# Optimization experiments

Measured on AMD Instinct MI355X. Metric: run time of the kernel, lower is better.

Reference implementation:

```python
import jax, jax.numpy as jnp
import numpy as np

N_TRAIN = 131072
M_TEST = 65536
T_SPAN = 100.0
D = 3  # Matern-5/2 state dim


def setup_inputs() -> dict:
    key = jax.random.key(0)
    k1, k2, k3, k4 = jax.random.split(key, 4)
    times = jnp.sort(jax.random.uniform(k1, (N_TRAIN,), jnp.float32) * T_SPAN)
    t_star = jnp.sort(jax.random.uniform(k2, (M_TEST,), jnp.float32) * T_SPAN)
    # positive site precisions, site naturals scaled so pseudo-targets are O(1)
    site_nat2 = jax.random.uniform(k3, (N_TRAIN,), jnp.float32) * 4.0 + 0.5
    site_nat1 = jax.random.normal(k4, (N_TRAIN,), jnp.float32) * site_nat2
    return dict(
        times=times,
        t_star=t_star,
        site_nat1=site_nat1,
        site_nat2=site_nat2,
        variance=jnp.float32(1.0),
        lengthscale=jnp.float32(0.5),
        mean_const=jnp.float32(0.1),
    )


def _matern52_sde(variance, lengthscale):
    lam = jnp.sqrt(5.0).astype(jnp.float32) / lengthscale
    F = jnp.array([[0.0, 1.0, 0.0],
                   [0.0, 0.0, 1.0],
                   [0.0, 0.0, 0.0]], jnp.float32)
    F = F.at[2, 0].set(-lam ** 3).at[2, 1].set(-3.0 * lam ** 2).at[2, 2].set(-3.0 * lam)
    kappa = lam ** 2 / 3.0
    P_inf = variance * jnp.array([[1.0, 0.0, 0.0],
                                  [0.0, 0.0, 0.0],
                                  [0.0, 0.0, 0.0]], jnp.float32)
    P_inf = P_inf.at[0, 2].set(-variance * kappa)
    P_inf = P_inf.at[2, 0].set(-variance * kappa)
    P_inf = P_inf.at[1, 1].set(variance * kappa)
    P_inf = P_inf.at[2, 2].set(variance * lam ** 4)
    H = jnp.array([[1.0, 0.0, 0.0]], jnp.float32)
    return F, H, P_inf, lam


def _discretise(F, P_inf, lam, dt):
    # (F + lam I) is nilpotent of index 3 -> exact expm
    I = jnp.eye(D, dtype=jnp.float32)
    Nm = F + lam * I
    Nm2 = Nm @ Nm
    dt_ = dt[:, None, None]
    A = jnp.exp(-lam * dt)[:, None, None] * (I + dt_ * Nm + 0.5 * dt_ ** 2 * Nm2)
    APA = jnp.einsum('tij,jk,tlk->til', A, P_inf, A)
    Q = P_inf - APA
    return A, Q


def _kalman_filter(H, P_inf, A_seq, Q_seq, residual, is_obs, R_full):
    h = H[0]  # [D]

    def step(carry, inp):
        m, P = carry
        A, Q, r, obs, R = inp
        m_pred = A @ m
        P_pred = A @ P @ A.T + Q
        S = h @ P_pred @ h + R
        K = obs * (P_pred @ h) / S  # masked gain: test points skip update
        v = r - m_pred @ h
        m_f = m_pred + K * v
        P_f = P_pred - jnp.outer(K, K) * S
        return (m_f, P_f), (m_pred, P_pred, m_f, P_f)

    init = (jnp.zeros(D, jnp.float32), P_inf)
    _, (m_pred, P_pred, m_filt, P_filt) = jax.lax.scan(
        step, init, (A_seq, Q_seq, residual, is_obs, R_full))
    return m_pred, P_pred, m_filt, P_filt


def _rts_smoother(m_pred, P_pred, m_filt, P_filt, A_seq):
    def back(carry, inp):
        m_s_next, P_s_next = carry
        m_f, P_f, A_n, m_p_n, P_p_n = inp
        G = jnp.linalg.solve(P_p_n, A_n @ P_f).T  # P_f A^T P_pred^{-1}
        m_s = m_f + G @ (m_s_next - m_p_n)
        P_s = P_f + G @ (P_s_next - P_p_n) @ G.T
        return (m_s, P_s), (m_s, P_s)

    init = (m_filt[-1], P_filt[-1])
    xs = (m_filt[:-1], P_filt[:-1], A_seq[1:], m_pred[1:], P_pred[1:])
    _, (m_s, P_s) = jax.lax.scan(back, init, xs, reverse=True)
    m_smooth = jnp.concatenate([m_s, m_filt[-1:]], axis=0)
    P_smooth = jnp.concatenate([P_s, P_filt[-1:]], axis=0)
    return m_smooth, P_smooth


def reference(times, t_star, site_nat1, site_nat2, variance, lengthscale, mean_const):
    F, H, P_inf, lam = _matern52_sde(variance, lengthscale)
    N = times.shape[0]
    M = t_star.shape[0]
    merged = jnp.concatenate([times, t_star])
    order = jnp.argsort(merged)  # jnp.argsort is stable
    merged_sorted = merged[order]
    is_obs = jnp.concatenate([jnp.ones(N, jnp.float32), jnp.zeros(M, jnp.float32)])[order]
    pseudo_targets = site_nat1 / site_nat2
    residual_full = jnp.concatenate([pseudo_targets - mean_const,
                                     jnp.zeros(M, jnp.float32)])[order]
    R_full = jnp.concatenate([jnp.reciprocal(site_nat2), jnp.ones(M, jnp.float32)])[order]
    dt_full = jnp.concatenate([jnp.zeros(1, jnp.float32), jnp.diff(merged_sorted)])
    A_seq, Q_seq = _discretise(F, P_inf, lam, dt_full)
    m_pred, P_pred, m_filt, P_filt = _kalman_filter(
        H, P_inf, A_seq, Q_seq, residual_full, is_obs, R_full)
    m_smooth, P_smooth = _rts_smoother(m_pred, P_pred, m_filt, P_filt, A_seq)
    inv_order = jnp.argsort(order)
    test_positions = inv_order[N:]
    m_test = m_smooth[test_positions]
    P_test = P_smooth[test_positions]
    means = m_test @ H[0] + mean_const  # H = [1,0,0]
    vars_ = jnp.einsum('i,tij,j->t', H[0], P_test, H[0])
    return means, jnp.maximum(vars_, 0.0)
```

## Files before the change

kernel.cpp:

```cpp
#include <hip/hip_runtime.h>
#include <math.h>

#define DEV __device__ __forceinline__

constexpr int N_TRAIN = 131072;
constexpr int M_TEST  = 65536;
constexpr int T_TOT   = N_TRAIN + M_TEST;
constexpr int TPB     = 64;
constexpr int NBLK    = T_TOT / TPB;
constexpr int GRP     = 64;
constexpr int NGRP    = NBLK / GRP;
constexpr int FE_S    = 33;

DEV void mm(const float* X, const float* Y, float* Z) {
#pragma unroll
  for (int i = 0; i < 3; ++i)
#pragma unroll
    for (int j = 0; j < 3; ++j)
      Z[i*3+j] = X[i*3]*Y[j] + X[i*3+1]*Y[3+j] + X[i*3+2]*Y[6+j];
}
DEV void mmnt(const float* X, const float* Y, float* Z) {
#pragma unroll
  for (int i = 0; i < 3; ++i)
#pragma unroll
    for (int j = 0; j < 3; ++j)
      Z[i*3+j] = X[i*3]*Y[j*3] + X[i*3+1]*Y[j*3+1] + X[i*3+2]*Y[j*3+2];
}
DEV void mtn(const float* X, const float* Y, float* Z) {
#pragma unroll
  for (int i = 0; i < 3; ++i)
#pragma unroll
    for (int j = 0; j < 3; ++j)
      Z[i*3+j] = X[i]*Y[j] + X[3+i]*Y[3+j] + X[6+i]*Y[6+j];
}
DEV void mv(const float* X, const float* v, float* w) {
#pragma unroll
  for (int i = 0; i < 3; ++i) w[i] = X[i*3]*v[0] + X[i*3+1]*v[1] + X[i*3+2]*v[2];
}
DEV void mtv(const float* X, const float* v, float* w) {
#pragma unroll
  for (int i = 0; i < 3; ++i) w[i] = X[i]*v[0] + X[3+i]*v[1] + X[6+i]*v[2];
}
DEV void inv3(const float* mf_, float* o) {
  double m0=mf_[0], m1=mf_[1], m2=mf_[2], m3=mf_[3], m4=mf_[4],
         m5=mf_[5], m6=mf_[6], m7=mf_[7], m8=mf_[8];
  double c00 = m4*m8 - m5*m7;
  double c10 = m5*m6 - m3*m8;
  double c20 = m3*m7 - m4*m6;
  double det = m0*c00 + m1*c10 + m2*c20;
  double id = 1.0 / det;
  o[0] = (float)(c00*id); o[1] = (float)((m2*m7-m1*m8)*id); o[2] = (float)((m1*m5-m2*m4)*id);
  o[3] = (float)(c10*id); o[4] = (float)((m0*m8-m2*m6)*id); o[5] = (float)((m2*m3-m0*m5)*id);
  o[6] = (float)(c20*id); o[7] = (float)((m1*m6-m0*m7)*id); o[8] = (float)((m0*m4-m1*m3)*id);
}
DEV void symm(float* P) {
  float a = 0.5f*(P[1]+P[3]), b = 0.5f*(P[2]+P[6]), c = 0.5f*(P[5]+P[7]);
  P[1]=P[3]=a; P[2]=P[6]=b; P[5]=P[7]=c;
}

struct Model { float lam, v, kap, l4; };
DEV Model make_model(const float* varp, const float* ellp) {
  Model M; M.v = varp[0];
  float ell = ellp[0];
  M.lam = sqrtf(5.0f) / ell;
  M.kap = M.lam * M.lam / 3.0f;
  float l2 = M.lam * M.lam;
  M.l4 = l2 * l2;
  return M;
}
DEV void pinf(const Model& M, float* P) {
  float vk = M.v * M.kap;
  P[0]=M.v; P[1]=0;  P[2]=-vk;
  P[3]=0;   P[4]=vk; P[5]=0;
  P[6]=-vk; P[7]=0;  P[8]=M.v*M.l4;
}
DEV void make_AQ(const Model& M, float dt, float* A, float* Q) {
  float lam = M.lam, l2 = lam*lam, l3 = l2*lam, l4 = M.l4;
  float e = __expf(-lam * dt);
  float h = 0.5f * dt * dt;
  A[0] = e*(1.0f + dt*lam + h*l2);
  A[1] = e*(dt + 2.0f*h*lam);
  A[2] = e*h;
  A[3] = e*(-h*l3);
  A[4] = e*(1.0f + dt*lam - 2.0f*h*l2);
  A[5] = e*(dt - h*lam);
  A[6] = e*(-dt*l3 + h*l4);
  A[7] = e*(-3.0f*dt*l2 + 2.0f*h*l3);
  A[8] = e*(1.0f - 2.0f*dt*lam + h*l2);
  float vk = M.v * M.kap, vl4 = M.v * M.l4;
  float B[9];
#pragma unroll
  for (int i = 0; i < 3; ++i) {
    B[i*3+0] =  A[i*3+0]*M.v - A[i*3+2]*vk;
    B[i*3+1] =  A[i*3+1]*vk;
    B[i*3+2] = -A[i*3+0]*vk  + A[i*3+2]*vl4;
  }
  float Pi[9]; pinf(M, Pi);
#pragma unroll
  for (int i = 0; i < 3; ++i)
#pragma unroll
    for (int j = 0; j < 3; ++j)
      Q[i*3+j] = Pi[i*3+j] - (B[i*3]*A[j*3] + B[i*3+1]*A[j*3+1] + B[i*3+2]*A[j*3+2]);
}

struct FE { float A[9]; float b[3]; float C[9]; float h[3]; float J[9]; };

DEV FE fe_identity() {
  FE e;
#pragma unroll
  for (int i=0;i<9;++i){ e.A[i]=0.0f; e.C[i]=0.0f; e.J[i]=0.0f; }
  e.A[0]=e.A[4]=e.A[8]=1.0f;
  e.b[0]=e.b[1]=e.b[2]=0.0f; e.h[0]=e.h[1]=e.h[2]=0.0f;
  return e;
}
DEV void fe_store(const FE& e, float* g) {
#pragma unroll
  for (int i=0;i<9;++i) g[i]=e.A[i];
  g[9]=e.b[0]; g[10]=e.b[1]; g[11]=e.b[2];
#pragma unroll
  for (int i=0;i<9;++i) g[12+i]=e.C[i];
  g[21]=e.h[0]; g[22]=e.h[1]; g[23]=e.h[2];
#pragma unroll
  for (int i=0;i<9;++i) g[24+i]=e.J[i];
}
DEV FE fe_load(const float* g) {
  FE e;
#pragma unroll
  for (int i=0;i<9;++i) e.A[i]=g[i];
  e.b[0]=g[9]; e.b[1]=g[10]; e.b[2]=g[11];
#pragma unroll
  for (int i=0;i<9;++i) e.C[i]=g[12+i];
  e.h[0]=g[21]; e.h[1]=g[22]; e.h[2]=g[23];
#pragma unroll
  for (int i=0;i<9;++i) e.J[i]=g[24+i];
  return e;
}
DEV void fe_storeT(const FE& e, float* g, int idx, int n) {
#pragma unroll
  for (int i=0;i<9;++i) g[i*n+idx]=e.A[i];
#pragma unroll
  for (int i=0;i<3;++i) g[(9+i)*n+idx]=e.b[i];
#pragma unroll
  for (int i=0;i<9;++i) g[(12+i)*n+idx]=e.C[i];
#pragma unroll
  for (int i=0;i<3;++i) g[(21+i)*n+idx]=e.h[i];
#pragma unroll
  for (int i=0;i<9;++i) g[(24+i)*n+idx]=e.J[i];
}
DEV FE fe_loadT(const float* g, int idx, int n) {
  FE e;
#pragma unroll
  for (int i=0;i<9;++i) e.A[i]=g[i*n+idx];
#pragma unroll
  for (int i=0;i<3;++i) e.b[i]=g[(9+i)*n+idx];
#pragma unroll
  for (int i=0;i<9;++i) e.C[i]=g[(12+i)*n+idx];
#pragma unroll
  for (int i=0;i<3;++i) e.h[i]=g[(21+i)*n+idx];
#pragma unroll
  for (int i=0;i<9;++i) e.J[i]=g[(24+i)*n+idx];
  return e;
}
DEV FE fe_shfl_up(const FE& e, int d) {
  FE o;
#pragma unroll
  for (int i=0;i<9;++i) o.A[i]=__shfl_up(e.A[i], d, 64);
#pragma unroll
  for (int i=0;i<3;++i) o.b[i]=__shfl_up(e.b[i], d, 64);
#pragma unroll
  for (int i=0;i<9;++i) o.C[i]=__shfl_up(e.C[i], d, 64);
#pragma unroll
  for (int i=0;i<3;++i) o.h[i]=__shfl_up(e.h[i], d, 64);
#pragma unroll
  for (int i=0;i<9;++i) o.J[i]=__shfl_up(e.J[i], d, 64);
  return o;
}
DEV FE build_felem(const Model& M, float dt, float obsf, float rf, float Rf_, bool first) {
  FE E;
  float r = rf, R = Rf_;
  float g = (obsf > 0.5f) ? 1.0f : 0.0f;
  if (first) {
#pragma unroll
    for (int i=0;i<9;++i){ E.A[i]=0.0f; E.J[i]=0.0f; }
    E.h[0]=E.h[1]=E.h[2]=0.0f;
    float Pi[9]; pinf(M, Pi);
    float S = Pi[0] + R;
    float f = g / S;
    float K0=Pi[0]*f, K1=Pi[3]*f, K2=Pi[6]*f;
    E.b[0]=K0*r; E.b[1]=K1*r; E.b[2]=K2*r;
    E.C[0]=Pi[0]-S*K0*K0; E.C[1]=Pi[1]-S*K0*K1; E.C[2]=Pi[2]-S*K0*K2;
    E.C[3]=Pi[3]-S*K1*K0; E.C[4]=Pi[4]-S*K1*K1; E.C[5]=Pi[5]-S*K1*K2;
    E.C[6]=Pi[6]-S*K2*K0; E.C[7]=Pi[7]-S*K2*K1; E.C[8]=Pi[8]-S*K2*K2;
    return E;
  }
  float Am[9], Q[9]; make_AQ(M, dt, Am, Q);
  float S = Q[0] + R, iS = g / S;
  float K0=Q[0]*iS, K1=Q[3]*iS, K2=Q[6]*iS;
#pragma unroll
  for (int j = 0; j < 3; ++j) {
    E.A[j]   = Am[j]   - K0*Am[j];
    E.A[3+j] = Am[3+j] - K1*Am[j];
    E.A[6+j] = Am[6+j] - K2*Am[j];
    E.C[j]   = Q[j]    - K0*Q[j];
    E.C[3+j] = Q[3+j]  - K1*Q[j];
    E.C[6+j] = Q[6+j]  - K2*Q[j];
  }
  E.b[0]=K0*r; E.b[1]=K1*r; E.b[2]=K2*r;
  float riS = r*iS;
  E.h[0]=Am[0]*riS; E.h[1]=Am[1]*riS; E.h[2]=Am[2]*riS;
#pragma unroll
  for (int i = 0; i < 3; ++i)
#pragma unroll
    for (int j = 0; j < 3; ++j)
      E.J[i*3+j] = Am[i]*Am[j]*iS;
  return E;
}
DEV FE fcompose(const FE& x, const FE& y) {
  const float *A1=x.A,*b1=x.b,*C1=x.C,*h1=x.h,*J1=x.J;
  const float *A2=y.A,*b2=y.b,*C2=y.C,*h2=y.h,*J2=y.J;
  FE o;
  float Mx[9]; mm(C1,J2,Mx); Mx[0]+=1.0f; Mx[4]+=1.0f; Mx[8]+=1.0f;
  float Mi[9]; inv3(Mx,Mi);
  float T1[9]; mm(A2,Mi,T1);
  mm(T1,A1,o.A);
  float u[3]; mv(C1,h2,u); u[0]+=b1[0]; u[1]+=b1[1]; u[2]+=b1[2];
  mv(T1,u,o.b); o.b[0]+=b2[0]; o.b[1]+=b2[1]; o.b[2]+=b2[2];
  float t2[9]; mm(T1,C1,t2);
  mmnt(t2,A2,o.C);
#pragma unroll
  for (int i=0;i<9;++i) o.C[i]+=C2[i];
  float tmp[9]; mm(Mi,A1,tmp);
  float w[3]; mv(J2,b1,w);
  w[0]=h2[0]-w[0]; w[1]=h2[1]-w[1]; w[2]=h2[2]-w[2];
  mtv(tmp,w,o.h); o.h[0]+=h1[0]; o.h[1]+=h1[1]; o.h[2]+=h1[2];
  float V[9]; mm(J2,A1,V);
  mtn(tmp,V,o.J);
#pragma unroll
  for (int i=0;i<9;++i) o.J[i]+=J1[i];
  symm(o.C); symm(o.J);
  return o;
}
DEV void fstep(const Model& M, float dt, float obsf, float rf, float Rf_,
               float* m, float* P) {
  float A[9], Q[9]; make_AQ(M, dt, A, Q);
  float mp[3]; mv(A, m, mp);
  float W[9]; mmnt(P, A, W);
  float Pp[9]; mm(A, W, Pp);
#pragma unroll
  for (int i=0;i<9;++i) Pp[i]+=Q[i];
  float S = Pp[0] + Rf_;
  float f = (obsf > 0.5f) ? (1.0f/S) : 0.0f;
  float K0=Pp[0]*f, K1=Pp[3]*f, K2=Pp[6]*f;
  float v = rf - mp[0];
  m[0]=mp[0]+K0*v; m[1]=mp[1]+K1*v; m[2]=mp[2]+K2*v;
  P[0]=Pp[0]-S*K0*K0; P[1]=Pp[1]-S*K0*K1; P[2]=Pp[2]-S*K0*K2;
  P[3]=Pp[3]-S*K1*K0; P[4]=Pp[4]-S*K1*K1; P[5]=Pp[5]-S*K1*K2;
  P[6]=Pp[6]-S*K2*K0; P[7]=Pp[7]-S*K2*K1; P[8]=Pp[8]-S*K2*K2;
  symm(P);
}

struct SE { float G[9]; float c[3]; float U[9]; };

DEV SE se_identity() {
  SE s;
#pragma unroll
  for (int i=0;i<9;++i){ s.G[i]=0.0f; s.U[i]=0.0f; }
  s.G[0]=s.G[4]=s.G[8]=1.0f;
  s.c[0]=s.c[1]=s.c[2]=0.0f;
  return s;
}
DEV void se_store(const SE& s, float* g) {
#pragma unroll
  for (int i=0;i<9;++i) g[i]=s.G[i];
  g[9]=s.c[0]; g[10]=s.c[1]; g[11]=s.c[2];
  g[12]=s.U[0]; g[13]=s.U[1]; g[14]=s.U[2]; g[15]=s.U[4]; g[16]=s.U[5]; g[17]=s.U[8];
}
DEV SE se_load(const float* g) {
  SE s;
#pragma unroll
  for (int i=0;i<9;++i) s.G[i]=g[i];
  s.c[0]=g[9]; s.c[1]=g[10]; s.c[2]=g[11];
  s.U[0]=g[12]; s.U[1]=g[13]; s.U[2]=g[14];
  s.U[3]=g[13]; s.U[4]=g[15]; s.U[5]=g[16];
  s.U[6]=g[14]; s.U[7]=g[16]; s.U[8]=g[17];
  return s;
}
DEV void se_storeT(const SE& s, float* g, int idx, int n) {
#pragma unroll
  for (int i=0;i<9;++i) g[i*n+idx]=s.G[i];
#pragma unroll
  for (int i=0;i<3;++i) g[(9+i)*n+idx]=s.c[i];
  g[12*n+idx]=s.U[0]; g[13*n+idx]=s.U[1]; g[14*n+idx]=s.U[2];
  g[15*n+idx]=s.U[4]; g[16*n+idx]=s.U[5]; g[17*n+idx]=s.U[8];
}
DEV SE se_loadT(const float* g, int idx, int n) {
  SE s;
#pragma unroll
  for (int i=0;i<9;++i) s.G[i]=g[i*n+idx];
#pragma unroll
  for (int i=0;i<3;++i) s.c[i]=g[(9+i)*n+idx];
  float u0=g[12*n+idx], u1=g[13*n+idx], u2=g[14*n+idx],
        u4=g[15*n+idx], u5=g[16*n+idx], u8=g[17*n+idx];
  s.U[0]=u0; s.U[1]=u1; s.U[2]=u2;
  s.U[3]=u1; s.U[4]=u4; s.U[5]=u5;
  s.U[6]=u2; s.U[7]=u5; s.U[8]=u8;
  return s;
}
DEV SE se_shfl_down(const SE& s, int d) {
  SE o;
#pragma unroll
  for (int i=0;i<9;++i) o.G[i]=__shfl_down(s.G[i], d, 64);
#pragma unroll
  for (int i=0;i<3;++i) o.c[i]=__shfl_down(s.c[i], d, 64);
#pragma unroll
  for (int i=0;i<9;++i) o.U[i]=__shfl_down(s.U[i], d, 64);
  return o;
}
DEV SE scompose(const SE& x, const SE& y) {
  SE o;
  mm(x.G, y.G, o.G);
  float t[3]; mv(x.G, y.c, t);
  o.c[0]=t[0]+x.c[0]; o.c[1]=t[1]+x.c[1]; o.c[2]=t[2]+x.c[2];
  float T[9]; mm(x.G, y.U, T);
  mmnt(T, x.G, o.U);
#pragma unroll
  for (int i=0;i<9;++i) o.U[i]+=x.U[i];
  symm(o.U);
  return o;
}
DEV void sapply(const SE& s, float* m, float* P) {
  float t[3]; mv(s.G, m, t);
  float T[9]; mm(s.G, P, T);
  float Pn[9]; mmnt(T, s.G, Pn);
  m[0]=t[0]+s.c[0]; m[1]=t[1]+s.c[1]; m[2]=t[2]+s.c[2];
#pragma unroll
  for (int i=0;i<9;++i) P[i]=Pn[i]+s.U[i];
  symm(P);
}
DEV SE build_selem(const Model& M, const float4* pk, const float* mf, const float* Pf, int k) {
  float m[3] = { mf[k], mf[T_TOT+k], mf[2*T_TOT+k] };
  float p00=Pf[k], p01=Pf[T_TOT+k], p02=Pf[2*T_TOT+k],
        p11=Pf[3*T_TOT+k], p12=Pf[4*T_TOT+k], p22=Pf[5*T_TOT+k];
  float P[9] = { p00,p01,p02, p01,p11,p12, p02,p12,p22 };
  float dt = pk[k+1].x - pk[k].x;
  SE s;
  float A[9], Q[9]; make_AQ(M, dt, A, Q);
  float W[9]; mmnt(P, A, W);
  float Pp[9]; mm(A, W, Pp);
#pragma unroll
  for (int j=0;j<9;++j) Pp[j]+=Q[j];
  float Pi_[9]; inv3(Pp, Pi_);
  mm(W, Pi_, s.G);
  float mp[3]; mv(A, m, mp);
  float gm[3]; mv(s.G, mp, gm);
  s.c[0]=m[0]-gm[0]; s.c[1]=m[1]-gm[1]; s.c[2]=m[2]-gm[2];
  float GW[9]; mmnt(s.G, W, GW);
#pragma unroll
  for (int j=0;j<9;++j) s.U[j]=P[j]-GW[j];
  symm(s.U);
  return s;
}

__global__ void k_merge(const float* __restrict__ times, const float* __restrict__ tstar,
                        const float* __restrict__ n1, const float* __restrict__ n2,
                        const float* __restrict__ mcp,
                        float4* pk, int* oix) {
  int g = blockIdx.x*blockDim.x + threadIdx.x;
  if (g >= T_TOT) return;
  float mc = mcp[0];
  if (g < N_TRAIN) {
    int i = g;
    float t = times[i];
    int lo = 0, hi = M_TEST;
    while (lo < hi) { int mid=(lo+hi)>>1; if (tstar[mid] < t) lo=mid+1; else hi=mid; }
    int p = i + lo;
    float s2 = n2[i];
    pk[p] = make_float4(t, n1[i]/s2 - mc, 1.0f/s2, 1.0f);
    oix[p] = -1;
  } else {
    int j = g - N_TRAIN;
    float t = tstar[j];
    int lo = 0, hi = N_TRAIN;
    while (lo < hi) { int mid=(lo+hi)>>1; if (times[mid] <= t) lo=mid+1; else hi=mid; }
    int p = j + lo;
    pk[p] = make_float4(t, 0.f, 1.f, 0.f);
    oix[p] = j;
  }
}

__global__ __launch_bounds__(TPB, 3) void k_f1(
    const float* varp, const float* ellp, const float4* __restrict__ pk,
    float* tIncl, float* blkAgg) {
  int l = threadIdx.x, b = blockIdx.x;
  int t = b*TPB + l;
  Model M = make_model(varp, ellp);
  float4 q = pk[t];
  float dt = (t == 0) ? 0.0f : (q.x - pk[t-1].x);
  FE run = build_felem(M, dt, q.w, q.y, q.z, t == 0);
  for (int d = 1; d < TPB; d <<= 1) {
    FE oth = fe_shfl_up(run, d);
    FE comp = fcompose(oth, run);
    if (l >= d) run = comp;
  }
  fe_storeT(run, tIncl, t, T_TOT);
  if (l == TPB-1) fe_storeT(run, blkAgg, b, NBLK);
}

__global__ __launch_bounds__(TPB, 2) void k_f2a(const float* __restrict__ blkAgg,
                                                float* blkIncl2, float* grpAgg) {
  int l = threadIdx.x, gb = blockIdx.x;
  int b = gb*GRP + l;
  FE run = fe_loadT(blkAgg, b, NBLK);
  for (int d = 1; d < TPB; d <<= 1) {
    FE oth = fe_shfl_up(run, d);
    FE comp = fcompose(oth, run);
    if (l >= d) run = comp;
  }
  fe_storeT(run, blkIncl2, b, NBLK);
  if (l == GRP-1) fe_store(run, grpAgg + gb*FE_S);
}

__global__ __launch_bounds__(TPB, 2) void k_f2b(const float* __restrict__ grpAgg,
                                                float* grpPref) {
  int j = threadIdx.x;
  FE run = (j < NGRP) ? fe_load(grpAgg + j*FE_S) : fe_identity();
  for (int d = 1; d < TPB; d <<= 1) {
    FE oth = fe_shfl_up(run, d);
    FE comp = fcompose(oth, run);
    if (j >= d) run = comp;
  }
  FE X = fe_shfl_up(run, 1);
  if (j < NGRP) {
    if (j == 0) X = fe_identity();
    fe_store(X, grpPref + j*FE_S);
  }
}

__global__ __launch_bounds__(TPB, 3) void k_f3(
    const float* varp, const float* ellp, const float4* __restrict__ pk,
    const float* __restrict__ tIncl, const float* __restrict__ blkIncl2,
    const float* __restrict__ grpPref,
    float* mf, float* Pf, float* xT) {
  int l = threadIdx.x, b = blockIdx.x;
  int t = b*TPB + l;
  int g = b >> 6, lb = b & (GRP-1);
  Model M = make_model(varp, ellp);
  float m[3], P[9];
  if (t == 0) {
    m[0]=m[1]=m[2]=0.0f; pinf(M, P);
  } else {
    FE gp = fe_load(grpPref + g*FE_S);
    FE entB = (lb == 0) ? gp : fcompose(gp, fe_loadT(blkIncl2, b-1, NBLK));
    FE ent  = (l == 0) ? entB : fcompose(entB, fe_loadT(tIncl, t-1, T_TOT));
    m[0]=ent.b[0]; m[1]=ent.b[1]; m[2]=ent.b[2];
#pragma unroll
    for (int i=0;i<9;++i) P[i]=ent.C[i];
  }
  float4 q = pk[t];
  float dt = (t == 0) ? 0.0f : (q.x - pk[t-1].x);
  fstep(M, dt, q.w, q.y, q.z, m, P);
  mf[t]=m[0]; mf[T_TOT+t]=m[1]; mf[2*T_TOT+t]=m[2];
  Pf[t]=P[0]; Pf[T_TOT+t]=P[1]; Pf[2*T_TOT+t]=P[2];
  Pf[3*T_TOT+t]=P[4]; Pf[4*T_TOT+t]=P[5]; Pf[5*T_TOT+t]=P[8];
  if (t == T_TOT-1) {
    xT[0]=m[0]; xT[1]=m[1]; xT[2]=m[2];
    xT[3]=P[0]; xT[4]=P[1]; xT[5]=P[2];
    xT[6]=P[4]; xT[7]=P[5]; xT[8]=P[8];
  }
}

__global__ __launch_bounds__(TPB, 3) void k_s1(
    const float* varp, const float* ellp, const float4* __restrict__ pk,
    const float* __restrict__ mf, const float* __restrict__ Pf,
    float* eSel, float* tSuf, float* blkAggS) {
  int l = threadIdx.x, b = blockIdx.x;
  int t = b*TPB + l;
  Model M = make_model(varp, ellp);
  SE e = (t <= T_TOT-2) ? build_selem(M, pk, mf, Pf, t) : se_identity();
  se_storeT(e, eSel, t, T_TOT);
  SE Macc = e;
  for (int d = 1; d < TPB; d <<= 1) {
    SE oth = se_shfl_down(Macc, d);
    SE comp = scompose(Macc, oth);
    if (l + d < TPB) Macc = comp;
  }
  se_storeT(Macc, tSuf, t, T_TOT);
  if (l == 0) se_storeT(Macc, blkAggS, b, NBLK);
}

__global__ __launch_bounds__(TPB, 2) void k_s2a(const float* __restrict__ blkAggS,
                                                float* blkSuf2, float* grpAggS) {
  int l = threadIdx.x, gb = blockIdx.x;
  int b = gb*GRP + l;
  SE run = se_loadT(blkAggS, b, NBLK);
  for (int d = 1; d < TPB; d <<= 1) {
    SE oth = se_shfl_down(run, d);
    SE comp = scompose(run, oth);
    if (l + d < TPB) run = comp;
  }
  se_storeT(run, blkSuf2, b, NBLK);
  if (l == 0) se_store(run, grpAggS + gb*18);
}

__global__ __launch_bounds__(TPB, 2) void k_s2b(const float* __restrict__ grpAggS,
                                                const float* __restrict__ xT,
                                                float* gExit) {
  int j = threadIdx.x;
  SE run = (j < NGRP) ? se_load(grpAggS + j*18) : se_identity();
  for (int d = 1; d < TPB; d <<= 1) {
    SE oth = se_shfl_down(run, d);
    SE comp = scompose(run, oth);
    if (j + d < TPB) run = comp;
  }
  SE Sx = se_shfl_down(run, 1);
  if (j < NGRP) {
    float m[3] = { xT[0], xT[1], xT[2] };
    float P[9] = { xT[3],xT[4],xT[5], xT[4],xT[6],xT[7], xT[5],xT[7],xT[8] };
    if (j < NGRP-1) sapply(Sx, m, P);
    float* o = gExit + j*9;
    o[0]=m[0];o[1]=m[1];o[2]=m[2];o[3]=P[0];o[4]=P[1];o[5]=P[2];o[6]=P[4];o[7]=P[5];o[8]=P[8];
  }
}

__global__ __launch_bounds__(TPB, 4) void k_s3(
    const float* mcp,
    const float* __restrict__ eSel, const float* __restrict__ tSuf,
    const float* __restrict__ blkSuf2, const float* __restrict__ gExit,
    const int* __restrict__ oix, float* out) {
  int l = threadIdx.x, b = blockIdx.x;
  int t = b*TPB + l;
  int g = b >> 6, lb = b & (GRP-1);
  float mc = mcp[0];
  const float* ge = gExit + g*9;
  float m[3] = { ge[0], ge[1], ge[2] };
  float P[9] = { ge[3],ge[4],ge[5], ge[4],ge[6],ge[7], ge[5],ge[7],ge[8] };
  if (lb < GRP-1) {
    SE s = se_loadT(blkSuf2, b+1, NBLK);
    sapply(s, m, P);
  }
  if (l < TPB-1) {
    SE s = se_loadT(tSuf, t+1, T_TOT);
    sapply(s, m, P);
  }
  {
    SE e = se_loadT(eSel, t, T_TOT);
    sapply(e, m, P);
  }
  int j = oix[t];
  if (j >= 0) { out[j] = m[0] + mc; out[M_TEST + j] = fmaxf(P[0], 0.0f); }
}

extern "C" void kernel_launch(void* const* d_in, const int* in_sizes, int n_in,
                              void* d_out, int out_size, void* d_ws, size_t ws_size,
                              hipStream_t stream) {
  const float* times = (const float*)d_in[0];
  const float* tstar = (const float*)d_in[1];
  const float* n1    = (const float*)d_in[2];
  const float* n2    = (const float*)d_in[3];
  const float* varp  = (const float*)d_in[4];
  const float* ellp  = (const float*)d_in[5];
  const float* mcp   = (const float*)d_in[6];
  float* out = (float*)d_out;

  size_t off = 0;
  auto take = [&](size_t bytes) {
    char* p = (char*)d_ws + off;
    off += (bytes + 255) & ~(size_t)255;
    return (void*)p;
  };
  float4* pk     = (float4*)take(sizeof(float4) * T_TOT);
  int*    oix    = (int*)   take(sizeof(int)    * T_TOT);
  float*  mf     = (float*) take(sizeof(float)  * 3 * T_TOT);
  float*  Pf     = (float*) take(sizeof(float)  * 6 * T_TOT);
  float*  tIncl  = (float*) take(sizeof(float)  * FE_S * T_TOT);
  float*  blkAgg = (float*) take(sizeof(float)  * FE_S * NBLK);
  float*  blkIncl2=(float*) take(sizeof(float)  * FE_S * NBLK);
  float*  grpAgg = (float*) take(sizeof(float)  * FE_S * NGRP);
  float*  grpPref= (float*) take(sizeof(float)  * FE_S * NGRP);
  float*  eSel   = (float*) take(sizeof(float)  * 18 * T_TOT);
  float*  tSuf   = (float*) take(sizeof(float)  * 18 * T_TOT);
  float*  blkAggS= (float*) take(sizeof(float)  * 18 * NBLK);
  float*  blkSuf2= (float*) take(sizeof(float)  * 18 * NBLK);
  float*  grpAggS= (float*) take(sizeof(float)  * 18 * NGRP);
  float*  gExit  = (float*) take(sizeof(float)  * 9  * NGRP);
  float*  xT     = (float*) take(sizeof(float)  * 9);
  (void)ws_size; (void)in_sizes; (void)n_in; (void)out_size;

  k_merge<<<(T_TOT+255)/256, 256, 0, stream>>>(times, tstar, n1, n2, mcp, pk, oix);
  k_f1   <<<NBLK, TPB, 0, stream>>>(varp, ellp, pk, tIncl, blkAgg);
  k_f2a  <<<NGRP, TPB, 0, stream>>>(blkAgg, blkIncl2, grpAgg);
  k_f2b  <<<1, TPB, 0, stream>>>(grpAgg, grpPref);
  k_f3   <<<NBLK, TPB, 0, stream>>>(varp, ellp, pk, tIncl, blkIncl2, grpPref, mf, Pf, xT);
  k_s1   <<<NBLK, TPB, 0, stream>>>(varp, ellp, pk, mf, Pf, eSel, tSuf, blkAggS);
  k_s2a  <<<NGRP, TPB, 0, stream>>>(blkAggS, blkSuf2, grpAggS);
  k_s2b  <<<1, TPB, 0, stream>>>(grpAggS, xT, gExit);
  k_s3   <<<NBLK, TPB, 0, stream>>>(mcp, eSel, tSuf, blkSuf2, gExit, oix, out);
}
```

Baseline: 150.5 us.

## Fuse smoother element build into filter pass and apply prefixes to state directly

Smoother elements are now built inside the final filter kernel from the just-computed filtered state, so the filtered means and covariances are no longer written to and re-read from global memory by a separate kernel. The filter prefix is applied to the state vector with a cheaper apply routine instead of composing full elements, which avoids up to two full 3x3 compositions per thread. The final smoother step computes only the entries it needs for the mean and variance outputs. The 3x3 inverse inside element composition is switched from double to single precision, which may reduce numerical accuracy.

```diff
diff --git a/kernel.cpp b/kernel.cpp
--- a/kernel.cpp
+++ b/kernel.cpp
@@ -41,7 +41,17 @@
 #pragma unroll
   for (int i = 0; i < 3; ++i) w[i] = X[i]*v[0] + X[3+i]*v[1] + X[6+i]*v[2];
 }
-DEV void inv3(const float* mf_, float* o) {
+DEV void inv3f(const float* m, float* o) {
+  float c00 = m[4]*m[8] - m[5]*m[7];
+  float c10 = m[5]*m[6] - m[3]*m[8];
+  float c20 = m[3]*m[7] - m[4]*m[6];
+  float det = m[0]*c00 + m[1]*c10 + m[2]*c20;
+  float id = 1.0f / det;
+  o[0] = c00*id; o[1] = (m[2]*m[7]-m[1]*m[8])*id; o[2] = (m[1]*m[5]-m[2]*m[4])*id;
+  o[3] = c10*id; o[4] = (m[0]*m[8]-m[2]*m[6])*id; o[5] = (m[2]*m[3]-m[0]*m[5])*id;
+  o[6] = c20*id; o[7] = (m[1]*m[6]-m[0]*m[7])*id; o[8] = (m[0]*m[4]-m[1]*m[3])*id;
+}
+DEV void inv3d(const float* mf_, float* o) {
   double m0=mf_[0], m1=mf_[1], m2=mf_[2], m3=mf_[3], m4=mf_[4],
          m5=mf_[5], m6=mf_[6], m7=mf_[7], m8=mf_[8];
   double c00 = m4*m8 - m5*m7;
@@ -161,6 +171,12 @@
   for (int i=0;i<9;++i) e.J[i]=g[(24+i)*n+idx];
   return e;
 }
+DEV void fe_loadT_state(const float* g, int idx, int n, float* m, float* P) {
+#pragma unroll
+  for (int i=0;i<3;++i) m[i]=g[(9+i)*n+idx];
+#pragma unroll
+  for (int i=0;i<9;++i) P[i]=g[(12+i)*n+idx];
+}
 DEV FE fe_shfl_up(const FE& e, int d) {
   FE o;
 #pragma unroll
@@ -220,7 +236,7 @@
   const float *A2=y.A,*b2=y.b,*C2=y.C,*h2=y.h,*J2=y.J;
   FE o;
   float Mx[9]; mm(C1,J2,Mx); Mx[0]+=1.0f; Mx[4]+=1.0f; Mx[8]+=1.0f;
-  float Mi[9]; inv3(Mx,Mi);
+  float Mi[9]; inv3f(Mx,Mi);
   float T1[9]; mm(A2,Mi,T1);
   mm(T1,A1,o.A);
   float u[3]; mv(C1,h2,u); u[0]+=b1[0]; u[1]+=b1[1]; u[2]+=b1[2];
@@ -239,6 +255,19 @@
   for (int i=0;i<9;++i) o.J[i]+=J1[i];
   symm(o.C); symm(o.J);
   return o;
+}
+DEV void fapply(const FE& y, float* m, float* P) {
+  float Mx[9]; mm(P, y.J, Mx); Mx[0]+=1.0f; Mx[4]+=1.0f; Mx[8]+=1.0f;
+  float Mi[9]; inv3f(Mx, Mi);
+  float T1[9]; mm(y.A, Mi, T1);
+  float u[3]; mv(P, y.h, u); u[0]+=m[0]; u[1]+=m[1]; u[2]+=m[2];
+  float mn[3]; mv(T1, u, mn);
+  m[0]=mn[0]+y.b[0]; m[1]=mn[1]+y.b[1]; m[2]=mn[2]+y.b[2];
+  float t2[9]; mm(T1, P, t2);
+  float Pn[9]; mmnt(t2, y.A, Pn);
+#pragma unroll
+  for (int i=0;i<9;++i) P[i]=Pn[i]+y.C[i];
+  symm(P);
 }
 DEV void fstep(const Model& M, float dt, float obsf, float rf, float Rf_,
                float* m, float* P) {
@@ -337,19 +366,14 @@
   for (int i=0;i<9;++i) P[i]=Pn[i]+s.U[i];
   symm(P);
 }
-DEV SE build_selem(const Model& M, const float4* pk, const float* mf, const float* Pf, int k) {
-  float m[3] = { mf[k], mf[T_TOT+k], mf[2*T_TOT+k] };
-  float p00=Pf[k], p01=Pf[T_TOT+k], p02=Pf[2*T_TOT+k],
-        p11=Pf[3*T_TOT+k], p12=Pf[4*T_TOT+k], p22=Pf[5*T_TOT+k];
-  float P[9] = { p00,p01,p02, p01,p11,p12, p02,p12,p22 };
-  float dt = pk[k+1].x - pk[k].x;
+DEV SE selem_from_state(const Model& M, const float* m, const float* P, float dtn) {
   SE s;
-  float A[9], Q[9]; make_AQ(M, dt, A, Q);
+  float A[9], Q[9]; make_AQ(M, dtn, A, Q);
   float W[9]; mmnt(P, A, W);
   float Pp[9]; mm(A, W, Pp);
 #pragma unroll
   for (int j=0;j<9;++j) Pp[j]+=Q[j];
-  float Pi_[9]; inv3(Pp, Pi_);
+  float Pi_[9]; inv3d(Pp, Pi_);
   mm(W, Pi_, s.G);
   float mp[3]; mv(A, m, mp);
   float gm[3]; mv(s.G, mp, gm);
@@ -440,7 +464,7 @@
     const float* varp, const float* ellp, const float4* __restrict__ pk,
     const float* __restrict__ tIncl, const float* __restrict__ blkIncl2,
     const float* __restrict__ grpPref,
-    float* mf, float* Pf, float* xT) {
+    float* eSel, float* xT) {
   int l = threadIdx.x, b = blockIdx.x;
   int t = b*TPB + l;
   int g = b >> 6, lb = b & (GRP-1);
@@ -448,37 +472,41 @@
   float m[3], P[9];
   if (t == 0) {
     m[0]=m[1]=m[2]=0.0f; pinf(M, P);
+  } else if (g == 0 && lb == 0) {
+    fe_loadT_state(tIncl, t-1, T_TOT, m, P);
+  } else if (g == 0) {
+    fe_loadT_state(blkIncl2, b-1, NBLK, m, P);
+    if (l > 0) { FE y = fe_loadT(tIncl, t-1, T_TOT); fapply(y, m, P); }
   } else {
-    FE gp = fe_load(grpPref + g*FE_S);
-    FE entB = (lb == 0) ? gp : fcompose(gp, fe_loadT(blkIncl2, b-1, NBLK));
-    FE ent  = (l == 0) ? entB : fcompose(entB, fe_loadT(tIncl, t-1, T_TOT));
-    m[0]=ent.b[0]; m[1]=ent.b[1]; m[2]=ent.b[2];
-#pragma unroll
-    for (int i=0;i<9;++i) P[i]=ent.C[i];
+    const float* gp = grpPref + g*FE_S;
+    m[0]=gp[9]; m[1]=gp[10]; m[2]=gp[11];
+#pragma unroll
+    for (int i=0;i<9;++i) P[i]=gp[12+i];
+    if (lb > 0) { FE y = fe_loadT(blkIncl2, b-1, NBLK); fapply(y, m, P); }
+    if (l  > 0) { FE y = fe_loadT(tIncl,  t-1, T_TOT); fapply(y, m, P); }
   }
   float4 q = pk[t];
   float dt = (t == 0) ? 0.0f : (q.x - pk[t-1].x);
   fstep(M, dt, q.w, q.y, q.z, m, P);
-  mf[t]=m[0]; mf[T_TOT+t]=m[1]; mf[2*T_TOT+t]=m[2];
-  Pf[t]=P[0]; Pf[T_TOT+t]=P[1]; Pf[2*T_TOT+t]=P[2];
-  Pf[3*T_TOT+t]=P[4]; Pf[4*T_TOT+t]=P[5]; Pf[5*T_TOT+t]=P[8];
-  if (t == T_TOT-1) {
+  SE e;
+  if (t < T_TOT-1) {
+    float dtn = pk[t+1].x - q.x;
+    e = selem_from_state(M, m, P, dtn);
+  } else {
+    e = se_identity();
     xT[0]=m[0]; xT[1]=m[1]; xT[2]=m[2];
     xT[3]=P[0]; xT[4]=P[1]; xT[5]=P[2];
     xT[6]=P[4]; xT[7]=P[5]; xT[8]=P[8];
   }
-}
-
-__global__ __launch_bounds__(TPB, 3) void k_s1(
-    const float* varp, const float* ellp, const float4* __restrict__ pk,
-    const float* __restrict__ mf, const float* __restrict__ Pf,
-    float* eSel, float* tSuf, float* blkAggS) {
+  se_storeT(e, eSel, t, T_TOT);
+}
+
+__global__ __launch_bounds__(TPB, 4) void k_s1(
+    const float* __restrict__ eSel,
+    float* tSuf, float* blkAggS) {
   int l = threadIdx.x, b = blockIdx.x;
   int t = b*TPB + l;
-  Model M = make_model(varp, ellp);
-  SE e = (t <= T_TOT-2) ? build_selem(M, pk, mf, Pf, t) : se_identity();
-  se_storeT(e, eSel, t, T_TOT);
-  SE Macc = e;
+  SE Macc = se_loadT(eSel, t, T_TOT);
   for (int d = 1; d < TPB; d <<= 1) {
     SE oth = se_shfl_down(Macc, d);
     SE comp = scompose(Macc, oth);
@@ -542,12 +570,15 @@
     SE s = se_loadT(tSuf, t+1, T_TOT);
     sapply(s, m, P);
   }
-  {
-    SE e = se_loadT(eSel, t, T_TOT);
-    sapply(e, m, P);
-  }
+  float g0 = eSel[0*T_TOT+t], g1 = eSel[1*T_TOT+t], g2 = eSel[2*T_TOT+t];
+  float c0 = eSel[9*T_TOT+t], u00 = eSel[12*T_TOT+t];
+  float m0 = g0*m[0] + g1*m[1] + g2*m[2] + c0;
+  float p0 = g0*P[0] + g1*P[3] + g2*P[6];
+  float p1 = g0*P[1] + g1*P[4] + g2*P[7];
+  float p2 = g0*P[2] + g1*P[5] + g2*P[8];
+  float v00 = p0*g0 + p1*g1 + p2*g2 + u00;
   int j = oix[t];
-  if (j >= 0) { out[j] = m[0] + mc; out[M_TEST + j] = fmaxf(P[0], 0.0f); }
+  if (j >= 0) { out[j] = m0 + mc; out[M_TEST + j] = fmaxf(v00, 0.0f); }
 }
 
 extern "C" void kernel_launch(void* const* d_in, const int* in_sizes, int n_in,
@@ -570,8 +601,6 @@
   };
   float4* pk     = (float4*)take(sizeof(float4) * T_TOT);
   int*    oix    = (int*)   take(sizeof(int)    * T_TOT);
-  float*  mf     = (float*) take(sizeof(float)  * 3 * T_TOT);
-  float*  Pf     = (float*) take(sizeof(float)  * 6 * T_TOT);
   float*  tIncl  = (float*) take(sizeof(float)  * FE_S * T_TOT);
   float*  blkAgg = (float*) take(sizeof(float)  * FE_S * NBLK);
   float*  blkIncl2=(float*) take(sizeof(float)  * FE_S * NBLK);
@@ -590,8 +619,8 @@
   k_f1   <<<NBLK, TPB, 0, stream>>>(varp, ellp, pk, tIncl, blkAgg);
   k_f2a  <<<NGRP, TPB, 0, stream>>>(blkAgg, blkIncl2, grpAgg);
   k_f2b  <<<1, TPB, 0, stream>>>(grpAgg, grpPref);
-  k_f3   <<<NBLK, TPB, 0, stream>>>(varp, ellp, pk, tIncl, blkIncl2, grpPref, mf, Pf, xT);
-  k_s1   <<<NBLK, TPB, 0, stream>>>(varp, ellp, pk, mf, Pf, eSel, tSuf, blkAggS);
+  k_f3   <<<NBLK, TPB, 0, stream>>>(varp, ellp, pk, tIncl, blkIncl2, grpPref, eSel, xT);
+  k_s1   <<<NBLK, TPB, 0, stream>>>(eSel, tSuf, blkAggS);
   k_s2a  <<<NGRP, TPB, 0, stream>>>(blkAggS, blkSuf2, grpAggS);
   k_s2b  <<<1, TPB, 0, stream>>>(grpAggS, xT, gExit);
   k_s3   <<<NBLK, TPB, 0, stream>>>(mcp, eSel, tSuf, blkSuf2, gExit, oix, out);
```

Result: slower. 153.6 us (+2.0%).
